# Kernel optimization log

Hardware: AMD Instinct MI355X
Metric: run time of the kernel (lower is better)

Reference implementation:

```python
import jax, jax.numpy as jnp
import numpy as np

B, S, HID = 2, 2048, 2048
NH, NKV, D = 16, 4, 128  # heads, kv heads, dim_per_head
ROPE_BASE = 10000.0


def setup_inputs() -> dict:
    key = jax.random.key(0)
    ks = jax.random.split(key, 5)
    x = jax.random.normal(ks[0], (B, S, HID), jnp.float32)
    wq = jax.random.normal(ks[1], (HID, NH * D), jnp.float32) * 0.02
    wk = jax.random.normal(ks[2], (HID, NKV * D), jnp.float32) * 0.02
    wv = jax.random.normal(ks[3], (HID, NKV * D), jnp.float32) * 0.02
    wo = jax.random.normal(ks[4], (NH * D, HID), jnp.float32) * 0.02
    inv_freq = 1.0 / (ROPE_BASE ** (jnp.arange(0, D, 2, dtype=jnp.float32) / D))
    freqs = jnp.outer(jnp.arange(S, dtype=jnp.float32), inv_freq)  # [S, D/2]
    cos, sin = jnp.cos(freqs), jnp.sin(freqs)
    mask = jnp.tril(jnp.ones((S, S), dtype=bool))  # causal, True = attend
    return {"x": x, "wq": wq, "wk": wk, "wv": wv, "wo": wo,
            "cos": cos, "sin": sin, "mask": mask}


def _rope_interleave(t, cos, sin):
    # t: [B, H, S, D]; cos/sin: [S, D/2]; interleaved pairs (even, odd)
    te, to = t[..., ::2], t[..., 1::2]
    c, s = cos[None, None], sin[None, None]
    re = te * c - to * s
    ro = to * c + te * s
    return jnp.stack([re, ro], axis=-1).reshape(t.shape)


def reference(x, wq, wk, wv, wo, cos, sin, mask):
    b, s, _ = x.shape
    # QKV projections + shape(): [B, S, hid] -> [B, H, S, D]
    q = (x @ wq).reshape(b, s, NH, D).transpose(0, 2, 1, 3)
    k = (x @ wk).reshape(b, s, NKV, D).transpose(0, 2, 1, 3)
    v = (x @ wv).reshape(b, s, NKV, D).transpose(0, 2, 1, 3)
    q = _rope_interleave(q, cos, sin)
    k = _rope_interleave(k, cos, sin)
    # GQA: repeat each kv head heads//heads_kv times consecutively
    rep = NH // NKV
    k = jnp.repeat(k, rep, axis=1)
    v = jnp.repeat(v, rep, axis=1)
    scores = jnp.einsum('bhqd,bhkd->bhqk', q, k) * (D ** -0.5)
    scores = scores.astype(jnp.float32)
    scores = jnp.where(mask[None, None], scores, jnp.finfo(jnp.float32).min)
    attn = jax.nn.softmax(scores, axis=-1).astype(x.dtype)
    ctx = jnp.einsum('bhqk,bhkd->bhqd', attn, v)
    ctx = ctx.transpose(0, 2, 1, 3).reshape(b, s, NH * D)  # unshape()
    return ctx @ wo
```

## Files before the change

### kernel.cpp

```cpp
#include <hip/hip_runtime.h>
#include <hip/hip_bf16.h>
#include <math.h>

#define S_LEN 2048
#define HIDW 2048
#define NHEAD 16
#define NKVH 4
#define HD 128
#define NB 2
#define MROWS (NB * S_LEN)
#define QKVN (NHEAD * HD + 2 * NKVH * HD)
#define KOFF (NHEAD * HD)
#define VOFF (NHEAD * HD + NKVH * HD)

typedef __bf16 bf16_t;
typedef __bf16 bf16x4_t __attribute__((ext_vector_type(4)));
typedef __bf16 bf16x8_t __attribute__((ext_vector_type(8)));
typedef float f32x4_t __attribute__((ext_vector_type(4)));

__device__ __forceinline__ void gload_lds16(const bf16_t* g, bf16_t* l) {
  __builtin_amdgcn_global_load_lds(
      (const __attribute__((address_space(1))) void*)g,
      (__attribute__((address_space(3))) void*)l, 16, 0, 0);
}

__device__ __forceinline__ f32x4_t zero4() {
  f32x4_t z = {0.f, 0.f, 0.f, 0.f};
  return z;
}

__device__ __forceinline__ float fexp2(float x) {
#if __has_builtin(__builtin_amdgcn_exp2f)
  return __builtin_amdgcn_exp2f(x);
#else
  return exp2f(x);
#endif
}

__global__ __launch_bounds__(256) void k_cvt8(const float* __restrict__ in,
                                              bf16_t* __restrict__ out, int n8) {
  int i = blockIdx.x * 256 + threadIdx.x;
  if (i >= n8) return;
  const float4* p = (const float4*)(in + (size_t)i * 8);
  float4 a = p[0], b = p[1];
  bf16x8_t r;
  r[0] = (bf16_t)a.x; r[1] = (bf16_t)a.y; r[2] = (bf16_t)a.z; r[3] = (bf16_t)a.w;
  r[4] = (bf16_t)b.x; r[5] = (bf16_t)b.y; r[6] = (bf16_t)b.z; r[7] = (bf16_t)b.w;
  *(bf16x8_t*)(out + (size_t)i * 8) = r;
}

__global__ __launch_bounds__(256) void k_tr_cvt(const float* __restrict__ in,
                                                bf16_t* __restrict__ out, int R, int C) {
  __shared__ float t[32][33];
  int c0 = blockIdx.x * 32, r0 = blockIdx.y * 32;
  int tx = threadIdx.x & 31, ty = threadIdx.x >> 5;
#pragma unroll
  for (int rr = ty; rr < 32; rr += 8) t[rr][tx] = in[(size_t)(r0 + rr) * C + c0 + tx];
  __syncthreads();
#pragma unroll
  for (int rr = ty; rr < 32; rr += 8)
    out[(size_t)(c0 + rr) * R + r0 + tx] = (bf16_t)t[tx][rr];
}

template <int EPI, int BMH>
__global__ __launch_bounds__(512, 2) void k_gemm256(const bf16_t* __restrict__ A,
                                                    const bf16_t* __restrict__ Bt,
                                                    void* __restrict__ Cout,
                                                    int M, int N, int K, int nby,
                                                    const float* __restrict__ cosT,
                                                    const float* __restrict__ sinT,
                                                    bf16_t* __restrict__ vt) {
  __shared__ bf16_t As[2][BMH * 128 * 64];
  __shared__ bf16_t Bs[2][256 * 64];

  int tid = threadIdx.x;
  int lane = tid & 63, wid = tid >> 6;
  int l15 = lane & 15, lg = lane >> 4;
  int wrb = (wid >> 2) * (BMH * 64);
  int wcb = (wid & 3) * 64;

  int nwg = gridDim.x;
  int qx = nwg >> 3;
  int lin = blockIdx.x;
  int wg = (lin & 7) * qx + (lin >> 3);
  int row0 = (wg / nby) * (BMH * 128), col0 = (wg % nby) * 256;

  int srow = tid >> 3;
  int scol = ((tid & 7) ^ (srow & 7)) * 8;
  const bf16_t* Ag = A + (size_t)(row0 + srow) * K + scol;
  const bf16_t* Bg = Bt + (size_t)(col0 + srow) * K + scol;

  f32x4_t acc[BMH * 4][4];
#pragma unroll
  for (int i = 0; i < BMH * 4; i++)
#pragma unroll
    for (int j = 0; j < 4; j++) acc[i][j] = zero4();

  int xr = (l15 & 7) << 4;

#pragma unroll
  for (int u = 0; u < BMH * 2; u++)
    gload_lds16(Ag + (size_t)u * 64 * K, As[0] + u * 4096 + tid * 8);
#pragma unroll
  for (int u = 0; u < 4; u++)
    gload_lds16(Bg + (size_t)u * 64 * K, Bs[0] + u * 4096 + tid * 8);
  asm volatile("s_waitcnt vmcnt(0)" ::: "memory");
  __builtin_amdgcn_s_barrier();
  __builtin_amdgcn_sched_barrier(0);

  int nk = K >> 6;
  for (int t = 0; t < nk; t++) {
    int cur = t & 1;
    const char* Ac = (const char*)As[cur];
    const char* Bc = (const char*)Bs[cur];
    bf16_t* An = As[cur ^ 1];
    bf16_t* Bn = Bs[cur ^ 1];
    const bf16_t* Agn = Ag + (size_t)(t + 1) * 64;
    const bf16_t* Bgn = Bg + (size_t)(t + 1) * 64;
    bool pf = (t + 1 < nk);

    bf16x8_t af[4][2];
#pragma unroll
    for (int ph = 0; ph < 4; ph++) {
      const int mh = (BMH == 2) ? (ph >> 1) : 0;
      const int nh = (BMH == 2) ? (ph & 1) : ph;
      const int NJ = (BMH == 2) ? 2 : 1;
      if ((BMH == 2) ? (nh == 0) : (ph == 0)) {
#pragma unroll
        for (int i = 0; i < 4; i++) {
          int row = wrb + (mh * 4 + i) * 16 + l15;
#pragma unroll
          for (int kk = 0; kk < 2; kk++)
            af[i][kk] = *(const bf16x8_t*)(Ac + ((row * 128 + kk * 64 + lg * 16) ^ xr));
        }
      }
      bf16x8_t bfr[NJ][2];
#pragma unroll
      for (int j = 0; j < NJ; j++) {
        int rowb = wcb + (nh * NJ + j) * 16 + l15;
#pragma unroll
        for (int kk = 0; kk < 2; kk++)
          bfr[j][kk] = *(const bf16x8_t*)(Bc + ((rowb * 128 + kk * 64 + lg * 16) ^ xr));
      }
      if (pf) {
        if (BMH == 2) {
          if (ph == 0) {
            gload_lds16(Agn, An + tid * 8);
            gload_lds16(Agn + (size_t)64 * K, An + 4096 + tid * 8);
            gload_lds16(Bgn, Bn + tid * 8);
          } else if (ph == 1) {
            gload_lds16(Agn + (size_t)128 * K, An + 8192 + tid * 8);
            gload_lds16(Agn + (size_t)192 * K, An + 12288 + tid * 8);
            gload_lds16(Bgn + (size_t)64 * K, Bn + 4096 + tid * 8);
          } else if (ph == 2) {
            gload_lds16(Bgn + (size_t)128 * K, Bn + 8192 + tid * 8);
            gload_lds16(Bgn + (size_t)192 * K, Bn + 12288 + tid * 8);
          }
        } else {
          if (ph == 0) {
            gload_lds16(Agn, An + tid * 8);
            gload_lds16(Agn + (size_t)64 * K, An + 4096 + tid * 8);
          } else if (ph == 1) {
            gload_lds16(Bgn, Bn + tid * 8);
            gload_lds16(Bgn + (size_t)64 * K, Bn + 4096 + tid * 8);
          } else if (ph == 2) {
            gload_lds16(Bgn + (size_t)128 * K, Bn + 8192 + tid * 8);
            gload_lds16(Bgn + (size_t)192 * K, Bn + 12288 + tid * 8);
          }
        }
      }
      __builtin_amdgcn_s_barrier();
      __builtin_amdgcn_s_setprio(1);
#pragma unroll
      for (int i = 0; i < 4; i++)
#pragma unroll
        for (int j = 0; j < NJ; j++)
#pragma unroll
          for (int kk = 0; kk < 2; kk++)
            acc[mh * 4 + i][nh * NJ + j] = __builtin_amdgcn_mfma_f32_16x16x32_bf16(
                af[i][kk], bfr[j][kk], acc[mh * 4 + i][nh * NJ + j], 0, 0, 0);
      __builtin_amdgcn_s_setprio(0);
      if (ph < 3) __builtin_amdgcn_s_barrier();
    }
    if (pf) asm volatile("s_waitcnt vmcnt(0)" ::: "memory");
    __builtin_amdgcn_s_barrier();
    __builtin_amdgcn_sched_barrier(0);
  }

  if (EPI == 2) {
    const float QS = 0.08838834764831845f * 1.4426950408889634f;
#pragma unroll
    for (int i = 0; i < BMH * 4; i++) {
#pragma unroll
      for (int j = 0; j < 4; j++) {
        int c = col0 + wcb + j * 16 + l15;
        int rbase = row0 + wrb + i * 16 + lg * 4;
        if (c < VOFF) {
          float scale = (c < KOFF) ? QS : 1.0f;
          int p0 = (c & 127) >> 1;
          int codd = c & 1;
#pragma unroll
          for (int qd = 0; qd < 4; qd++) {
            int rr = rbase + qd;
            int s = rr & (S_LEN - 1);
            float self = acc[i][j][qd];
            float other = __shfl_xor(self, 1);
            float cv = cosT[s * 64 + p0], sv = sinT[s * 64 + p0];
            float outv = codd ? (self * cv + other * sv) : (self * cv - other * sv);
            ((bf16_t*)Cout)[(size_t)rr * N + c] = (bf16_t)(outv * scale);
          }
        } else {
          int dcol = c - VOFF;
          int kvh = dcol >> 7, d = dcol & 127;
          int bb = rbase >> 11;
          int sbase = rbase & (S_LEN - 1);
          bf16x4_t pk;
#pragma unroll
          for (int qd = 0; qd < 4; qd++) pk[qd] = (bf16_t)acc[i][j][qd];
          *(bf16x4_t*)(vt + ((size_t)((bb * NKVH + kvh) * HD + d)) * S_LEN + sbase) = pk;
        }
      }
    }
  } else {
#pragma unroll
    for (int i = 0; i < BMH * 4; i++) {
#pragma unroll
      for (int j = 0; j < 4; j++) {
        int r = row0 + wrb + i * 16 + lg * 4;
        int c = col0 + wcb + j * 16 + l15;
#pragma unroll
        for (int qd = 0; qd < 4; qd++)
          ((float*)Cout)[(size_t)(r + qd) * N + c] = acc[i][j][qd];
      }
    }
  }
}

__global__ __launch_bounds__(256, 2) void k_attn(const bf16_t* __restrict__ qkv,
                                                 const bf16_t* __restrict__ vt,
                                                 bf16_t* __restrict__ ctx) {
  __shared__ bf16_t Ks[2 * 64 * 128];
  __shared__ bf16_t Vs[2 * 128 * 64];
  __shared__ bf16_t plds[4][16 * 72];

  int tid = threadIdx.x;
  int lane = tid & 63, wid = tid >> 6;
  int idx = blockIdx.x;
  int bh = idx & 31;
  int qg = 31 - (idx >> 5);
  int b = bh >> 4, h = bh & 15;
  int kvh = h >> 2;
  int q0 = qg * 64 + wid * 16;
  int l15 = lane & 15, lg = lane >> 4;

  const bf16_t* Kbase = qkv + (size_t)(b * S_LEN) * QKVN + KOFF + kvh * HD;
  const bf16_t* Vbase = vt + (size_t)(b * NKVH + kvh) * HD * S_LEN;

  const bf16_t* Qp = qkv + (size_t)(b * S_LEN + q0 + l15) * QKVN + h * HD + lg * 8;
  bf16x8_t aq[4];
#pragma unroll
  for (int kk = 0; kk < 4; kk++) aq[kk] = *(const bf16x8_t*)(Qp + kk * 32);

  int Ls[4], Lk[4], Lv[4];
#pragma unroll
  for (int u = 0; u < 4; u++) {
    int L = u * 4096 + tid * 16;
    Ls[u] = L >> 1;
    Lk[u] = L ^ (((L >> 8) & 7) << 4);
    Lv[u] = L ^ (((L >> 7) & 7) << 4);
  }

  f32x4_t o[8];
#pragma unroll
  for (int j = 0; j < 8; j++) o[j] = zero4();
  float m[4], lsum[4];
#pragma unroll
  for (int i = 0; i < 4; i++) { m[i] = -INFINITY; lsum[i] = 0.f; }

  bf16_t* pbuf = &plds[wid][0];
  int xr = (l15 & 7) << 4;
  int ntiles = qg + 1;

#pragma unroll
  for (int u = 0; u < 4; u++) {
    gload_lds16(Kbase + (size_t)(Lk[u] >> 8) * QKVN + ((Lk[u] & 255) >> 1), Ks + Ls[u]);
    gload_lds16(Vbase + (size_t)(Lv[u] >> 7) * S_LEN + ((Lv[u] & 127) >> 1), Vs + Ls[u]);
  }
  __syncthreads();

  for (int t = 0; t < ntiles; t++) {
    int kv0 = t * 64;
    if (t + 1 < ntiles) {
      const bf16_t* Kn = Kbase + (size_t)(kv0 + 64) * QKVN;
      const bf16_t* Vn = Vbase + kv0 + 64;
      int bo = ((t + 1) & 1) * 8192;
#pragma unroll
      for (int u = 0; u < 4; u++) {
        gload_lds16(Kn + (size_t)(Lk[u] >> 8) * QKVN + ((Lk[u] & 255) >> 1), Ks + bo + Ls[u]);
        gload_lds16(Vn + (size_t)(Lv[u] >> 7) * S_LEN + ((Lv[u] & 127) >> 1), Vs + bo + Ls[u]);
      }
    }
    const char* Kb = (const char*)Ks + (t & 1) * 16384;
    const char* Vb = (const char*)Vs + (t & 1) * 16384;

    f32x4_t sacc[4];
#pragma unroll
    for (int cg = 0; cg < 4; cg++) sacc[cg] = zero4();
#pragma unroll
    for (int cg = 0; cg < 4; cg++) {
#pragma unroll
      for (int kk = 0; kk < 4; kk++) {
        int boff = ((cg * 16 + l15) * 256 + kk * 64 + lg * 16) ^ xr;
        bf16x8_t bk = *(const bf16x8_t*)(Kb + boff);
        sacc[cg] = __builtin_amdgcn_mfma_f32_16x16x32_bf16(aq[kk], bk, sacc[cg], 0, 0, 0);
      }
    }
    if (kv0 + 63 > q0) {
#pragma unroll
      for (int cg = 0; cg < 4; cg++) {
        int col = kv0 + cg * 16 + l15;
#pragma unroll
        for (int i = 0; i < 4; i++) {
          int row = q0 + lg * 4 + i;
          if (col > row) sacc[cg][i] = -1e30f;
        }
      }
    }
    float pmax[4];
#pragma unroll
    for (int i = 0; i < 4; i++) {
      float v = fmaxf(fmaxf(sacc[0][i], sacc[1][i]), fmaxf(sacc[2][i], sacc[3][i]));
      v = fmaxf(v, __shfl_xor(v, 1));
      v = fmaxf(v, __shfl_xor(v, 2));
      v = fmaxf(v, __shfl_xor(v, 4));
      v = fmaxf(v, __shfl_xor(v, 8));
      pmax[i] = v;
    }
    float dm = fmaxf(fmaxf(pmax[0] - m[0], pmax[1] - m[1]),
                     fmaxf(pmax[2] - m[2], pmax[3] - m[3]));
    if (__any(dm > 8.0f)) {
#pragma unroll
      for (int i = 0; i < 4; i++) {
        float nm = fmaxf(m[i], pmax[i]);
        float sc = fexp2(m[i] - nm);
        m[i] = nm;
        lsum[i] *= sc;
#pragma unroll
        for (int j = 0; j < 8; j++) o[j][i] *= sc;
      }
    }
#pragma unroll
    for (int cg = 0; cg < 4; cg++)
#pragma unroll
      for (int i = 0; i < 4; i++) sacc[cg][i] = fexp2(sacc[cg][i] - m[i]);
#pragma unroll
    for (int i = 0; i < 4; i++) {
      float s = sacc[0][i] + sacc[1][i] + sacc[2][i] + sacc[3][i];
      s += __shfl_xor(s, 1);
      s += __shfl_xor(s, 2);
      s += __shfl_xor(s, 4);
      s += __shfl_xor(s, 8);
      lsum[i] += s;
    }
#pragma unroll
    for (int cg = 0; cg < 4; cg++)
#pragma unroll
      for (int i = 0; i < 4; i++)
        pbuf[(lg * 4 + i) * 72 + cg * 16 + l15] = (bf16_t)sacc[cg][i];
    __builtin_amdgcn_wave_barrier();
    bf16x8_t pa0 = *(const bf16x8_t*)(pbuf + l15 * 72 + lg * 8);
    bf16x8_t pa1 = *(const bf16x8_t*)(pbuf + l15 * 72 + 32 + lg * 8);
    __builtin_amdgcn_wave_barrier();
#pragma unroll
    for (int j = 0; j < 8; j++) {
      int d = j * 16 + l15;
      int bo0 = (d * 128 + lg * 16) ^ xr;
      int bo1 = (d * 128 + 64 + lg * 16) ^ xr;
      o[j] = __builtin_amdgcn_mfma_f32_16x16x32_bf16(
          pa0, *(const bf16x8_t*)(Vb + bo0), o[j], 0, 0, 0);
      o[j] = __builtin_amdgcn_mfma_f32_16x16x32_bf16(
          pa1, *(const bf16x8_t*)(Vb + bo1), o[j], 0, 0, 0);
    }
    __syncthreads();
  }

  bf16_t* Cp = ctx + (size_t)(b * S_LEN + q0) * KOFF + h * HD;
#pragma unroll
  for (int i = 0; i < 4; i++) {
    float inv = 1.f / lsum[i];
    int row = lg * 4 + i;
#pragma unroll
    for (int j = 0; j < 8; j++)
      Cp[(size_t)row * KOFF + j * 16 + l15] = (bf16_t)(o[j][i] * inv);
  }
}

extern "C" void kernel_launch(void* const* d_in, const int* in_sizes, int n_in,
                              void* d_out, int out_size, void* d_ws, size_t ws_size,
                              hipStream_t stream) {
  const float* x = (const float*)d_in[0];
  const float* wq = (const float*)d_in[1];
  const float* wk = (const float*)d_in[2];
  const float* wv = (const float*)d_in[3];
  const float* wo = (const float*)d_in[4];
  const float* cosT = (const float*)d_in[5];
  const float* sinT = (const float*)d_in[6];

  bf16_t* xb = (bf16_t*)d_ws;
  bf16_t* wqkvT = xb + (size_t)MROWS * HIDW;
  bf16_t* woT = wqkvT + (size_t)QKVN * HIDW;
  bf16_t* qkv = woT + (size_t)HIDW * HIDW;
  bf16_t* vtb = qkv + (size_t)MROWS * QKVN;

  k_cvt8<<<MROWS * HIDW / 8 / 256, 256, 0, stream>>>(x, xb, MROWS * HIDW / 8);
  k_tr_cvt<<<dim3(KOFF / 32, HIDW / 32), 256, 0, stream>>>(wq, wqkvT, HIDW, KOFF);
  k_tr_cvt<<<dim3((NKVH * HD) / 32, HIDW / 32), 256, 0, stream>>>(
      wk, wqkvT + (size_t)KOFF * HIDW, HIDW, NKVH * HD);
  k_tr_cvt<<<dim3((NKVH * HD) / 32, HIDW / 32), 256, 0, stream>>>(
      wv, wqkvT + (size_t)VOFF * HIDW, HIDW, NKVH * HD);
  k_tr_cvt<<<dim3(HIDW / 32, KOFF / 32), 256, 0, stream>>>(wo, woT, KOFF, HIDW);
  k_gemm256<2, 2><<<(MROWS / 256) * (QKVN / 256), 512, 0, stream>>>(
      xb, wqkvT, qkv, MROWS, QKVN, HIDW, QKVN / 256, cosT, sinT, vtb);
  k_attn<<<32 * 32, 256, 0, stream>>>(qkv, vtb, xb);
  k_gemm256<0, 1><<<(MROWS / 128) * (HIDW / 256), 512, 0, stream>>>(
      xb, woT, d_out, MROWS, HIDW, KOFF, HIDW / 256, nullptr, nullptr, nullptr);
}
```

Before: 232.8 us.

## Stage RoPE cos/sin tables in LDS and move V transpose to separate kernel

In the QKV GEMM epilogue, the cos/sin rows for the block's 256 sequence positions are now bulk-loaded into the freed A/B shared-memory buffers with global_load_lds. The RoPE rotation then reads them from LDS instead of issuing scattered per-element global loads. The strided transposed V store in the epilogue is removed: V is written row-major into qkv, and a new 32x32 tiled transpose kernel builds vt. This replaces uncoalesced epilogue traffic with an extra kernel launch and an extra read and write of V.

```diff
diff --git a/kernel.cpp b/kernel.cpp
--- a/kernel.cpp
+++ b/kernel.cpp
@@ -68,8 +68,7 @@
                                                     void* __restrict__ Cout,
                                                     int M, int N, int K, int nby,
                                                     const float* __restrict__ cosT,
-                                                    const float* __restrict__ sinT,
-                                                    bf16_t* __restrict__ vt) {
+                                                    const float* __restrict__ sinT) {
   __shared__ bf16_t As[2][BMH * 128 * 64];
   __shared__ bf16_t Bs[2][256 * 64];
 
@@ -188,36 +187,52 @@
   }
 
   if (EPI == 2) {
-    const float QS = 0.08838834764831845f * 1.4426950408889634f;
-#pragma unroll
-    for (int i = 0; i < BMH * 4; i++) {
-#pragma unroll
-      for (int j = 0; j < 4; j++) {
-        int c = col0 + wcb + j * 16 + l15;
-        int rbase = row0 + wrb + i * 16 + lg * 4;
-        if (c < VOFF) {
+    if (col0 < VOFF) {
+      int sbase = row0 & (S_LEN - 1);
+      bf16_t* cosL = &As[0][0];
+      bf16_t* sinL = &Bs[0][0];
+#pragma unroll
+      for (int k = 0; k < 8; k++) {
+        gload_lds16((const bf16_t*)(cosT + (size_t)sbase * 64 + k * 2048 + tid * 4),
+                    cosL + k * 4096 + tid * 8);
+        gload_lds16((const bf16_t*)(sinT + (size_t)sbase * 64 + k * 2048 + tid * 4),
+                    sinL + k * 4096 + tid * 8);
+      }
+      asm volatile("s_waitcnt vmcnt(0)" ::: "memory");
+      __builtin_amdgcn_s_barrier();
+      const float* cosF = (const float*)cosL;
+      const float* sinF = (const float*)sinL;
+      const float QS = 0.08838834764831845f * 1.4426950408889634f;
+#pragma unroll
+      for (int i = 0; i < BMH * 4; i++) {
+#pragma unroll
+        for (int j = 0; j < 4; j++) {
+          int c = col0 + wcb + j * 16 + l15;
+          int rlb = wrb + i * 16 + lg * 4;
           float scale = (c < KOFF) ? QS : 1.0f;
           int p0 = (c & 127) >> 1;
           int codd = c & 1;
 #pragma unroll
           for (int qd = 0; qd < 4; qd++) {
-            int rr = rbase + qd;
-            int s = rr & (S_LEN - 1);
+            int rl = rlb + qd;
             float self = acc[i][j][qd];
             float other = __shfl_xor(self, 1);
-            float cv = cosT[s * 64 + p0], sv = sinT[s * 64 + p0];
+            float cv = cosF[rl * 64 + p0], sv = sinF[rl * 64 + p0];
             float outv = codd ? (self * cv + other * sv) : (self * cv - other * sv);
-            ((bf16_t*)Cout)[(size_t)rr * N + c] = (bf16_t)(outv * scale);
+            ((bf16_t*)Cout)[(size_t)(row0 + rl) * N + c] = (bf16_t)(outv * scale);
           }
-        } else {
-          int dcol = c - VOFF;
-          int kvh = dcol >> 7, d = dcol & 127;
-          int bb = rbase >> 11;
-          int sbase = rbase & (S_LEN - 1);
-          bf16x4_t pk;
-#pragma unroll
-          for (int qd = 0; qd < 4; qd++) pk[qd] = (bf16_t)acc[i][j][qd];
-          *(bf16x4_t*)(vt + ((size_t)((bb * NKVH + kvh) * HD + d)) * S_LEN + sbase) = pk;
+        }
+      }
+    } else {
+#pragma unroll
+      for (int i = 0; i < BMH * 4; i++) {
+#pragma unroll
+        for (int j = 0; j < 4; j++) {
+          int r = row0 + wrb + i * 16 + lg * 4;
+          int c = col0 + wcb + j * 16 + l15;
+#pragma unroll
+          for (int qd = 0; qd < 4; qd++)
+            ((bf16_t*)Cout)[(size_t)(r + qd) * N + c] = (bf16_t)acc[i][j][qd];
         }
       }
     }
@@ -234,6 +249,23 @@
       }
     }
   }
+}
+
+__global__ __launch_bounds__(256) void k_vt(const bf16_t* __restrict__ qkv,
+                                            bf16_t* __restrict__ vt) {
+  __shared__ bf16_t t[32][33];
+  int s0 = blockIdx.x * 32;
+  int dt = (blockIdx.y & 3) * 32;
+  int h = blockIdx.y >> 2;
+  int b = blockIdx.z;
+  int tx = threadIdx.x & 31, ty = threadIdx.x >> 5;
+#pragma unroll
+  for (int rr = ty; rr < 32; rr += 8)
+    t[rr][tx] = qkv[(size_t)(b * S_LEN + s0 + rr) * QKVN + VOFF + h * HD + dt + tx];
+  __syncthreads();
+#pragma unroll
+  for (int rr = ty; rr < 32; rr += 8)
+    vt[((size_t)((b * NKVH + h) * HD + dt + rr)) * S_LEN + s0 + tx] = t[tx][rr];
 }
 
 __global__ __launch_bounds__(256, 2) void k_attn(const bf16_t* __restrict__ qkv,
@@ -420,8 +452,9 @@
       wv, wqkvT + (size_t)VOFF * HIDW, HIDW, NKVH * HD);
   k_tr_cvt<<<dim3(HIDW / 32, KOFF / 32), 256, 0, stream>>>(wo, woT, KOFF, HIDW);
   k_gemm256<2, 2><<<(MROWS / 256) * (QKVN / 256), 512, 0, stream>>>(
-      xb, wqkvT, qkv, MROWS, QKVN, HIDW, QKVN / 256, cosT, sinT, vtb);
+      xb, wqkvT, qkv, MROWS, QKVN, HIDW, QKVN / 256, cosT, sinT);
+  k_vt<<<dim3(S_LEN / 32, 4 * NKVH, NB), 256, 0, stream>>>(qkv, vtb);
   k_attn<<<32 * 32, 256, 0, stream>>>(qkv, vtb, xb);
   k_gemm256<0, 1><<<(MROWS / 128) * (HIDW / 256), 512, 0, stream>>>(
-      xb, woT, d_out, MROWS, HIDW, KOFF, HIDW / 256, nullptr, nullptr, nullptr);
-}
+      xb, woT, d_out, MROWS, HIDW, KOFF, HIDW / 256, nullptr, nullptr);
+}
```

Result: no change. 234.4 us (+0.6%).
